# Kernel tuning notes

Measured on AMD Instinct MI355X. Metric: run time of the kernel, lower is better.

The kernel has to match this reference:

```python
import jax, jax.numpy as jnp
import numpy as np

N_NODES = 100000
N_EDGES = 1600000
D_IN = 64
D_OUT = 64


def setup_inputs() -> dict:
    key = jax.random.key(0)
    k1, k2, k3, k4, k5, k6 = jax.random.split(key, 6)
    feat = jax.random.normal(k1, (N_NODES, D_IN), dtype=jnp.float32)
    src = jax.random.randint(k2, (N_EDGES,), 0, N_NODES, dtype=jnp.int64)
    dst = jax.random.randint(k3, (N_EDGES,), 0, N_NODES, dtype=jnp.int64)
    edge_weight = jax.random.uniform(k4, (N_EDGES,), dtype=jnp.float32)
    # Xavier-uniform with relu gain, as in reset_parameters
    gain = float(np.sqrt(2.0))
    bound = gain * float(np.sqrt(6.0 / (D_IN + D_OUT)))
    W_neigh = jax.random.uniform(k5, (D_OUT, D_IN), dtype=jnp.float32, minval=-bound, maxval=bound)
    W_self = jax.random.uniform(k6, (D_OUT, D_IN), dtype=jnp.float32, minval=-bound, maxval=bound)
    bias = jnp.zeros((D_OUT,), dtype=jnp.float32)
    return {"feat": feat, "src": src, "dst": dst, "edge_weight": edge_weight,
            "W_neigh": W_neigh, "W_self": W_self, "bias": bias}


def reference(feat, src, dst, edge_weight, W_neigh, W_self, bias):
    n = feat.shape[0]
    # feat_drop with p=0.0 is identity; in_feats == out_feats so lin_before_mp is False
    # message: u_mul_e -> gather src features, scale by edge weight  [E, D_IN]
    m = feat[src] * edge_weight[:, None]
    # mean reduce over incoming edges (zero for isolated dst nodes, matching DGL)
    s = jax.ops.segment_sum(m, dst, num_segments=n)
    deg = jax.ops.segment_sum(jnp.ones_like(edge_weight), dst, num_segments=n)
    neigh = s / jnp.maximum(deg, 1.0)[:, None]
    h_neigh = neigh @ W_neigh.T
    h_self = feat @ W_self.T
    return h_self + h_neigh + bias
```

## Files before the change

kernel.cpp:

```cpp
#include <hip/hip_runtime.h>

constexpr int N_NODES = 100000;
constexpr int N_EDGES = 1600000;
constexpr int D = 64;

constexpr int BSH    = 7;
constexpr int BNODES = 1 << BSH;
constexpr int NBUCK  = (N_NODES + BNODES - 1) / BNODES;
constexpr int NPART  = 200;
constexpr int EPB    = N_EDGES / NPART;
constexpr int CAP    = 4096;

constexpr size_t OFF_BCNT    = 0;
constexpr size_t OFF_CURSOR  = 4096;
constexpr size_t OFF_BSTART  = 8192;
constexpr size_t OFF_STARTS  = 16384;
constexpr size_t OFF_ENTRIES = 425984;
constexpr size_t OFF_W16     = 13500416;
constexpr size_t OFF_AGG16   = 14680064;
constexpr size_t OFF_FEAT16  = 27480064;
constexpr size_t WS_NEEDED   = OFF_FEAT16 + (size_t)N_NODES * D * 2;

typedef short  bf16x8 __attribute__((ext_vector_type(8)));
typedef float  f32x4  __attribute__((ext_vector_type(4)));

__device__ __forceinline__ unsigned short f2bf(float f) {
    unsigned u = __float_as_uint(f);
    u += 0x7fffu + ((u >> 16) & 1u);
    return (unsigned short)(u >> 16);
}

__global__ __launch_bounds__(256) void k_cvt(const float4* __restrict__ feat4,
                                             unsigned short* __restrict__ feat16,
                                             const float* __restrict__ Wn,
                                             const float* __restrict__ Ws,
                                             unsigned short* __restrict__ W16) {
    const int i = blockIdx.x * 256 + threadIdx.x;
    float4 v = feat4[i];
    ushort4 o;
    o.x = f2bf(v.x); o.y = f2bf(v.y); o.z = f2bf(v.z); o.w = f2bf(v.w);
    *(ushort4*)&feat16[(size_t)i * 4] = o;
    if (blockIdx.x == 0) {
        for (int e = threadIdx.x; e < D * 128; e += 256) {
            const int j = e >> 7, k = e & 127;
            const float w = (k < D) ? Ws[j * D + k] : Wn[j * D + (k - D)];
            W16[e] = f2bf(w);
        }
    }
}

__global__ __launch_bounds__(256) void k_zero(int* __restrict__ bcnt) {
    int i = blockIdx.x * 256 + threadIdx.x;
    if (i < NBUCK) bcnt[i] = 0;
}

__global__ __launch_bounds__(256) void k_bcount(const int* __restrict__ dst,
                                                int* __restrict__ bcnt) {
    __shared__ int l[NBUCK];
    const int tid  = threadIdx.x;
    const int base = blockIdx.x * EPB;
    for (int i = tid; i < NBUCK; i += 256) l[i] = 0;
    __syncthreads();
    for (int k = tid; k < EPB; k += 256)
        atomicAdd(&l[dst[base + k] >> BSH], 1);
    __syncthreads();
    for (int b = tid; b < NBUCK; b += 256)
        if (l[b]) atomicAdd(&bcnt[b], l[b]);
}

__global__ __launch_bounds__(1024) void k_scan(const int* __restrict__ bcnt,
                                               int* __restrict__ bstart,
                                               int* __restrict__ cursor,
                                               int* __restrict__ starts) {
    __shared__ int s[1024];
    const int tid = threadIdx.x;
    const int v = (tid < NBUCK) ? bcnt[tid] : 0;
    s[tid] = v;
    __syncthreads();
    for (int off = 1; off < 1024; off <<= 1) {
        int u = (tid >= off) ? s[tid - off] : 0;
        __syncthreads();
        s[tid] += u;
        __syncthreads();
    }
    const int excl = s[tid] - v;
    if (tid <= NBUCK) bstart[tid] = excl;
    if (tid < NBUCK)  cursor[tid] = excl;
    if (tid == 0)     starts[N_NODES] = N_EDGES;
}

__global__ __launch_bounds__(256) void k_part(const int* __restrict__ src,
                                              const int* __restrict__ dst,
                                              const float* __restrict__ ew,
                                              int* __restrict__ cursor,
                                              uint2* __restrict__ entries) {
    __shared__ int l[NBUCK];
    const int tid  = threadIdx.x;
    const int base = blockIdx.x * EPB;
    for (int i = tid; i < NBUCK; i += 256) l[i] = 0;
    __syncthreads();
    for (int k = tid; k < EPB; k += 256)
        atomicAdd(&l[dst[base + k] >> BSH], 1);
    __syncthreads();
    for (int b = tid; b < NBUCK; b += 256) {
        const int c = l[b];
        l[b] = c ? atomicAdd(&cursor[b], c) : 0;
    }
    __syncthreads();
    for (int k = tid; k < EPB; k += 256) {
        const int e = base + k;
        const int d = dst[e];
        const int pos = atomicAdd(&l[d >> BSH], 1);
        entries[pos] = make_uint2((unsigned)src[e] | ((unsigned)(d & (BNODES - 1)) << 17),
                                  __float_as_uint(ew[e]));
    }
}

__global__ __launch_bounds__(256) void k_sort(uint2* __restrict__ entries,
                                              const int* __restrict__ bstart,
                                              int* __restrict__ starts) {
    __shared__ uint2 ent[CAP];
    __shared__ int h[BNODES];
    __shared__ int sc[BNODES];
    __shared__ int cur[BNODES];
    const int tid = threadIdx.x;
    const int b   = blockIdx.x;
    const int s0  = bstart[b];
    const int s1  = bstart[b + 1];
    const int cnt = (s1 - s0 <= CAP) ? (s1 - s0) : CAP;

    for (int i = tid; i < BNODES; i += 256) h[i] = 0;
    __syncthreads();
    for (int i = tid; i < cnt; i += 256) {
        uint2 e = entries[s0 + i];
        ent[i] = e;
        atomicAdd(&h[(e.x >> 17) & (BNODES - 1)], 1);
    }
    __syncthreads();
    if (tid < BNODES) sc[tid] = h[tid];
    __syncthreads();
    for (int off = 1; off < BNODES; off <<= 1) {
        int u = 0;
        if (tid < BNODES && tid >= off) u = sc[tid - off];
        __syncthreads();
        if (tid < BNODES) sc[tid] += u;
        __syncthreads();
    }
    if (tid < BNODES) {
        const int excl = sc[tid] - h[tid];
        cur[tid] = excl;
        const int node = (b << BSH) + tid;
        if (node < N_NODES) starts[node] = s0 + excl;
    }
    __syncthreads();
    for (int i = tid; i < cnt; i += 256) {
        uint2 e = ent[i];
        const int pos = atomicAdd(&cur[(e.x >> 17) & (BNODES - 1)], 1);
        entries[s0 + pos] = e;
    }
}

__global__ __launch_bounds__(256) void k_agg(const uint2* __restrict__ feat16u2,
                                             const int* __restrict__ starts,
                                             const uint2* __restrict__ entries,
                                             uint2* __restrict__ agg16u2) {
    const int wave = threadIdx.x >> 6;
    const int lane = threadIdx.x & 63;
    const int n = blockIdx.x * 4 + wave;
    if (n >= N_NODES) return;
    const int group = lane >> 4;
    const int gl    = lane & 15;
    const int s0 = starts[n];
    const int s1 = starts[n + 1];

    float4 acc = make_float4(0.f, 0.f, 0.f, 0.f);
    for (int e = s0 + group; e < s1; e += 4) {
        const uint2 en = entries[e];
        const float w  = __uint_as_float(en.y);
        const uint2 p  = feat16u2[(size_t)(en.x & 0x1FFFF) * 16 + gl];
        acc.x = fmaf(__uint_as_float(p.x << 16),          w, acc.x);
        acc.y = fmaf(__uint_as_float(p.x & 0xFFFF0000u),  w, acc.y);
        acc.z = fmaf(__uint_as_float(p.y << 16),          w, acc.z);
        acc.w = fmaf(__uint_as_float(p.y & 0xFFFF0000u),  w, acc.w);
    }
#pragma unroll
    for (int m = 16; m <= 32; m <<= 1) {
        acc.x += __shfl_xor(acc.x, m);
        acc.y += __shfl_xor(acc.y, m);
        acc.z += __shfl_xor(acc.z, m);
        acc.w += __shfl_xor(acc.w, m);
    }
    if (group == 0) {
        const float inv = 1.0f / fmaxf((float)(s1 - s0), 1.0f);
        uint2 o;
        o.x = (unsigned)f2bf(acc.x * inv) | ((unsigned)f2bf(acc.y * inv) << 16);
        o.y = (unsigned)f2bf(acc.z * inv) | ((unsigned)f2bf(acc.w * inv) << 16);
        agg16u2[(size_t)n * 16 + gl] = o;
    }
}

__global__ __launch_bounds__(256) void k_final(const unsigned short* __restrict__ feat16,
                                               const unsigned short* __restrict__ agg16,
                                               const unsigned short* __restrict__ W16,
                                               const float* __restrict__ bias,
                                               float* __restrict__ out) {
    const int tid  = threadIdx.x;
    const int wave = tid >> 6, lane = tid & 63;
    const int quad = lane >> 4, r = lane & 15;
    const int node0 = blockIdx.x * 64 + wave * 16;
    int arow = node0 + r;
    if (arow > N_NODES - 1) arow = N_NODES - 1;

    bf16x8 a[4], b[4][4];
    a[0] = *(const bf16x8*)&feat16[(size_t)arow * 64 +      quad * 8];
    a[1] = *(const bf16x8*)&feat16[(size_t)arow * 64 + 32 + quad * 8];
    a[2] = *(const bf16x8*)&agg16 [(size_t)arow * 64 +      quad * 8];
    a[3] = *(const bf16x8*)&agg16 [(size_t)arow * 64 + 32 + quad * 8];
#pragma unroll
    for (int nt = 0; nt < 4; ++nt)
#pragma unroll
        for (int kc = 0; kc < 4; ++kc)
            b[nt][kc] = *(const bf16x8*)&W16[(size_t)(nt * 16 + r) * 128 + kc * 32 + quad * 8];

    f32x4 acc[4] = {};
#pragma unroll
    for (int kc = 0; kc < 4; ++kc)
#pragma unroll
        for (int nt = 0; nt < 4; ++nt)
            acc[nt] = __builtin_amdgcn_mfma_f32_16x16x32_bf16(a[kc], b[nt][kc], acc[nt], 0, 0, 0);

#pragma unroll
    for (int nt = 0; nt < 4; ++nt) {
        const float bv = bias[nt * 16 + r];
#pragma unroll
        for (int reg = 0; reg < 4; ++reg) {
            const int m = node0 + quad * 4 + reg;
            if (m < N_NODES) out[(size_t)m * 64 + nt * 16 + r] = acc[nt][reg] + bv;
        }
    }
}

__global__ __launch_bounds__(256) void fb_zero(float4* __restrict__ out4,
                                               float* __restrict__ deg) {
    const int stride = gridDim.x * blockDim.x;
    int i = blockIdx.x * blockDim.x + threadIdx.x;
    const int total4 = (N_NODES * D) / 4;
    for (int idx = i; idx < total4; idx += stride)
        out4[idx] = make_float4(0.f, 0.f, 0.f, 0.f);
    for (int idx = i; idx < N_NODES; idx += stride)
        deg[idx] = 0.f;
}

__global__ __launch_bounds__(256) void fb_scatter(
    const float* __restrict__ feat, const int* __restrict__ src,
    const int* __restrict__ dst, const float* __restrict__ ew,
    float* __restrict__ out, float* __restrict__ deg) {
    const int gid  = blockIdx.x * blockDim.x + threadIdx.x;
    const int e    = gid >> 6;
    const int lane = gid & 63;
    if (e >= N_EDGES) return;
    atomicAdd(&out[(size_t)dst[e] * D + lane], feat[(size_t)src[e] * D + lane] * ew[e]);
    if (lane == 0) atomicAdd(&deg[dst[e]], 1.0f);
}

__global__ __launch_bounds__(256) void fb_finalize(
    const float* __restrict__ feat, const float* __restrict__ Wn,
    const float* __restrict__ Ws, const float* __restrict__ bias,
    const float* __restrict__ deg, float* __restrict__ out) {
    __shared__ float lWn[D * 65];
    __shared__ float lWs[D * 65];
    for (int idx = threadIdx.x; idx < D * D; idx += 256) {
        const int r = idx >> 6, c = idx & 63;
        lWn[r * 65 + c] = Wn[idx];
        lWs[r * 65 + c] = Ws[idx];
    }
    __syncthreads();
    const int wave = threadIdx.x >> 6;
    const int lane = threadIdx.x & 63;
    const int n = blockIdx.x * 4 + wave;
    if (n >= N_NODES) return;
    const float f  = feat[(size_t)n * D + lane];
    const float sv = out[(size_t)n * D + lane];
    const float inv = 1.0f / fmaxf(deg[n], 1.0f);
    float acc_s = 0.f, acc_n = 0.f;
#pragma unroll
    for (int k = 0; k < D; ++k) {
        acc_s += __shfl(f, k)  * lWs[lane * 65 + k];
        acc_n += __shfl(sv, k) * lWn[lane * 65 + k];
    }
    out[(size_t)n * D + lane] = acc_s + acc_n * inv + bias[lane];
}

extern "C" void kernel_launch(void* const* d_in, const int* in_sizes, int n_in,
                              void* d_out, int out_size, void* d_ws, size_t ws_size,
                              hipStream_t stream) {
    const float* feat = (const float*)d_in[0];
    const int*   src  = (const int*)  d_in[1];
    const int*   dst  = (const int*)  d_in[2];
    const float* ew   = (const float*)d_in[3];
    const float* Wn   = (const float*)d_in[4];
    const float* Ws   = (const float*)d_in[5];
    const float* bias = (const float*)d_in[6];
    float* out = (float*)d_out;
    char* ws = (char*)d_ws;

    if (ws_size >= WS_NEEDED) {
        int*   bcnt    = (int*)(ws + OFF_BCNT);
        int*   cursor  = (int*)(ws + OFF_CURSOR);
        int*   bstart  = (int*)(ws + OFF_BSTART);
        int*   starts  = (int*)(ws + OFF_STARTS);
        uint2* entries = (uint2*)(ws + OFF_ENTRIES);
        unsigned short* W16    = (unsigned short*)(ws + OFF_W16);
        unsigned short* agg16  = (unsigned short*)(ws + OFF_AGG16);
        unsigned short* feat16 = (unsigned short*)(ws + OFF_FEAT16);

        k_cvt   <<<(N_NODES * D / 4 + 255) / 256, 256, 0, stream>>>(
                    (const float4*)feat, feat16, Wn, Ws, W16);
        k_zero  <<<(NBUCK + 255) / 256, 256, 0, stream>>>(bcnt);
        k_bcount<<<NPART, 256, 0, stream>>>(dst, bcnt);
        k_scan  <<<1, 1024, 0, stream>>>(bcnt, bstart, cursor, starts);
        k_part  <<<NPART, 256, 0, stream>>>(src, dst, ew, cursor, entries);
        k_sort  <<<NBUCK, 256, 0, stream>>>(entries, bstart, starts);
        k_agg   <<<(N_NODES + 3) / 4, 256, 0, stream>>>((const uint2*)feat16, starts,
                                                        entries, (uint2*)agg16);
        k_final <<<(N_NODES + 63) / 64, 256, 0, stream>>>(feat16, agg16, W16, bias, out);
    } else {
        float* deg = (float*)d_ws;
        fb_zero<<<2048, 256, 0, stream>>>((float4*)out, deg);
        fb_scatter<<<(N_EDGES * 64) / 256, 256, 0, stream>>>(feat, src, dst, ew, out, deg);
        fb_finalize<<<(N_NODES + 3) / 4, 256, 0, stream>>>(feat, Wn, Ws, bias, deg, out);
    }
}
```

Measured before the change: 249.1 us.

## Fuse bucket sort, aggregation and output GEMM into one per-bucket kernel

Buckets shrink to 64 destination nodes. One kernel now sorts each bucket's edges in shared memory, aggregates neighbour features into a shared-memory bf16 row buffer and runs the MFMA projection directly from it. This removes the separate sort, aggregate and final kernels along with the global round trips for sorted entries, per-node starts and the agg16 buffer. The feature conversion, weight conversion and bucket count are also merged into one launch. The trade-off is that each block processes 16 nodes per wave serially, which may lower parallelism, and the shared buffer now caps a bucket at 2048 edges.

```diff
diff --git a/kernel.cpp b/kernel.cpp
--- a/kernel.cpp
+++ b/kernel.cpp
@@ -4,25 +4,26 @@
 constexpr int N_EDGES = 1600000;
 constexpr int D = 64;
 
-constexpr int BSH    = 7;
-constexpr int BNODES = 1 << BSH;
-constexpr int NBUCK  = (N_NODES + BNODES - 1) / BNODES;
+constexpr int BSH    = 6;
+constexpr int BN     = 1 << BSH;
+constexpr int NBUCK  = (N_NODES + BN - 1) / BN;
 constexpr int NPART  = 200;
 constexpr int EPB    = N_EDGES / NPART;
-constexpr int CAP    = 4096;
+constexpr int CAP    = 2048;
+constexpr int NCVT   = (N_NODES * D / 4) / 256;
 
 constexpr size_t OFF_BCNT    = 0;
-constexpr size_t OFF_CURSOR  = 4096;
-constexpr size_t OFF_BSTART  = 8192;
-constexpr size_t OFF_STARTS  = 16384;
-constexpr size_t OFF_ENTRIES = 425984;
-constexpr size_t OFF_W16     = 13500416;
-constexpr size_t OFF_AGG16   = 14680064;
-constexpr size_t OFF_FEAT16  = 27480064;
+constexpr size_t OFF_CURSOR  = 8192;
+constexpr size_t OFF_BSTART  = 16384;
+constexpr size_t OFF_ENTRIES = 24576;
+constexpr size_t OFF_W16     = 24576 + (size_t)N_EDGES * 8;
+constexpr size_t OFF_FEAT16  = 12845056;
 constexpr size_t WS_NEEDED   = OFF_FEAT16 + (size_t)N_NODES * D * 2;
 
 typedef short  bf16x8 __attribute__((ext_vector_type(8)));
 typedef float  f32x4  __attribute__((ext_vector_type(4)));
+
+union FragU { unsigned u[4]; bf16x8 v; };
 
 __device__ __forceinline__ unsigned short f2bf(float f) {
     unsigned u = __float_as_uint(f);
@@ -30,18 +31,38 @@
     return (unsigned short)(u >> 16);
 }
 
-__global__ __launch_bounds__(256) void k_cvt(const float4* __restrict__ feat4,
+__global__ __launch_bounds__(256) void k_zero(int* __restrict__ bcnt) {
+    int i = blockIdx.x * 256 + threadIdx.x;
+    if (i < NBUCK) bcnt[i] = 0;
+}
+
+__global__ __launch_bounds__(256) void k_pre(const float4* __restrict__ feat4,
                                              unsigned short* __restrict__ feat16,
                                              const float* __restrict__ Wn,
                                              const float* __restrict__ Ws,
-                                             unsigned short* __restrict__ W16) {
-    const int i = blockIdx.x * 256 + threadIdx.x;
-    float4 v = feat4[i];
-    ushort4 o;
-    o.x = f2bf(v.x); o.y = f2bf(v.y); o.z = f2bf(v.z); o.w = f2bf(v.w);
-    *(ushort4*)&feat16[(size_t)i * 4] = o;
-    if (blockIdx.x == 0) {
-        for (int e = threadIdx.x; e < D * 128; e += 256) {
+                                             unsigned short* __restrict__ W16,
+                                             const int* __restrict__ dst,
+                                             int* __restrict__ bcnt) {
+    __shared__ int l[NBUCK];
+    const int b   = blockIdx.x;
+    const int tid = threadIdx.x;
+    if (b < NCVT) {
+        const int i = b * 256 + tid;
+        float4 v = feat4[i];
+        ushort4 o;
+        o.x = f2bf(v.x); o.y = f2bf(v.y); o.z = f2bf(v.z); o.w = f2bf(v.w);
+        *(ushort4*)&feat16[(size_t)i * 4] = o;
+    } else if (b < NCVT + NPART) {
+        const int base = (b - NCVT) * EPB;
+        for (int i = tid; i < NBUCK; i += 256) l[i] = 0;
+        __syncthreads();
+        for (int k = tid; k < EPB; k += 256)
+            atomicAdd(&l[dst[base + k] >> BSH], 1);
+        __syncthreads();
+        for (int i = tid; i < NBUCK; i += 256)
+            if (l[i]) atomicAdd(&bcnt[i], l[i]);
+    } else {
+        for (int e = tid; e < D * 128; e += 256) {
             const int j = e >> 7, k = e & 127;
             const float w = (k < D) ? Ws[j * D + k] : Wn[j * D + (k - D)];
             W16[e] = f2bf(w);
@@ -49,44 +70,27 @@
     }
 }
 
-__global__ __launch_bounds__(256) void k_zero(int* __restrict__ bcnt) {
-    int i = blockIdx.x * 256 + threadIdx.x;
-    if (i < NBUCK) bcnt[i] = 0;
-}
-
-__global__ __launch_bounds__(256) void k_bcount(const int* __restrict__ dst,
-                                                int* __restrict__ bcnt) {
-    __shared__ int l[NBUCK];
-    const int tid  = threadIdx.x;
-    const int base = blockIdx.x * EPB;
-    for (int i = tid; i < NBUCK; i += 256) l[i] = 0;
-    __syncthreads();
-    for (int k = tid; k < EPB; k += 256)
-        atomicAdd(&l[dst[base + k] >> BSH], 1);
-    __syncthreads();
-    for (int b = tid; b < NBUCK; b += 256)
-        if (l[b]) atomicAdd(&bcnt[b], l[b]);
-}
-
 __global__ __launch_bounds__(1024) void k_scan(const int* __restrict__ bcnt,
                                                int* __restrict__ bstart,
-                                               int* __restrict__ cursor,
-                                               int* __restrict__ starts) {
+                                               int* __restrict__ cursor) {
     __shared__ int s[1024];
-    const int tid = threadIdx.x;
-    const int v = (tid < NBUCK) ? bcnt[tid] : 0;
-    s[tid] = v;
+    const int t  = threadIdx.x;
+    const int i0 = 2 * t, i1 = 2 * t + 1;
+    const int c0 = (i0 < NBUCK) ? bcnt[i0] : 0;
+    const int c1 = (i1 < NBUCK) ? bcnt[i1] : 0;
+    const int v  = c0 + c1;
+    s[t] = v;
     __syncthreads();
     for (int off = 1; off < 1024; off <<= 1) {
-        int u = (tid >= off) ? s[tid - off] : 0;
-        __syncthreads();
-        s[tid] += u;
-        __syncthreads();
-    }
-    const int excl = s[tid] - v;
-    if (tid <= NBUCK) bstart[tid] = excl;
-    if (tid < NBUCK)  cursor[tid] = excl;
-    if (tid == 0)     starts[N_NODES] = N_EDGES;
+        int u = (t >= off) ? s[t - off] : 0;
+        __syncthreads();
+        s[t] += u;
+        __syncthreads();
+    }
+    const int excl = s[t] - v;
+    if (i0 < NBUCK) { bstart[i0] = excl;      cursor[i0] = excl; }
+    if (i1 < NBUCK) { bstart[i1] = excl + c0; cursor[i1] = excl + c0; }
+    if (t == 0) bstart[NBUCK] = N_EDGES;
 }
 
 __global__ __launch_bounds__(256) void k_part(const int* __restrict__ src,
@@ -111,123 +115,116 @@
         const int e = base + k;
         const int d = dst[e];
         const int pos = atomicAdd(&l[d >> BSH], 1);
-        entries[pos] = make_uint2((unsigned)src[e] | ((unsigned)(d & (BNODES - 1)) << 17),
+        entries[pos] = make_uint2((unsigned)src[e] | ((unsigned)(d & (BN - 1)) << 17),
                                   __float_as_uint(ew[e]));
     }
 }
 
-__global__ __launch_bounds__(256) void k_sort(uint2* __restrict__ entries,
-                                              const int* __restrict__ bstart,
-                                              int* __restrict__ starts) {
+__global__ __launch_bounds__(256) void k_bucket(const uint2* __restrict__ feat16u2,
+                                                const unsigned short* __restrict__ feat16,
+                                                const int* __restrict__ bstart,
+                                                const uint2* __restrict__ entries,
+                                                const unsigned short* __restrict__ W16,
+                                                const float* __restrict__ bias,
+                                                float* __restrict__ out) {
     __shared__ uint2 ent[CAP];
-    __shared__ int h[BNODES];
-    __shared__ int sc[BNODES];
-    __shared__ int cur[BNODES];
+    __shared__ __align__(16) uint2 aggrow[BN * 16];
+    __shared__ int hh[BN], st[BN], cur[BN];
     const int tid = threadIdx.x;
     const int b   = blockIdx.x;
     const int s0  = bstart[b];
-    const int s1  = bstart[b + 1];
-    const int cnt = (s1 - s0 <= CAP) ? (s1 - s0) : CAP;
-
-    for (int i = tid; i < BNODES; i += 256) h[i] = 0;
+    int cnt = bstart[b + 1] - s0;
+    if (cnt > CAP) cnt = CAP;
+
+    if (tid < BN) hh[tid] = 0;
+    __syncthreads();
+    for (int i = tid; i < cnt; i += 256)
+        atomicAdd(&hh[(entries[s0 + i].x >> 17) & (BN - 1)], 1);
+    __syncthreads();
+    if (tid < BN) st[tid] = hh[tid];
+    __syncthreads();
+    for (int off = 1; off < BN; off <<= 1) {
+        int u = 0;
+        if (tid < BN && tid >= off) u = st[tid - off];
+        __syncthreads();
+        if (tid < BN) st[tid] += u;
+        __syncthreads();
+    }
+    if (tid < BN) { const int e0 = st[tid] - hh[tid]; st[tid] = e0; cur[tid] = e0; }
     __syncthreads();
     for (int i = tid; i < cnt; i += 256) {
         uint2 e = entries[s0 + i];
-        ent[i] = e;
-        atomicAdd(&h[(e.x >> 17) & (BNODES - 1)], 1);
-    }
-    __syncthreads();
-    if (tid < BNODES) sc[tid] = h[tid];
-    __syncthreads();
-    for (int off = 1; off < BNODES; off <<= 1) {
-        int u = 0;
-        if (tid < BNODES && tid >= off) u = sc[tid - off];
-        __syncthreads();
-        if (tid < BNODES) sc[tid] += u;
-        __syncthreads();
-    }
-    if (tid < BNODES) {
-        const int excl = sc[tid] - h[tid];
-        cur[tid] = excl;
-        const int node = (b << BSH) + tid;
-        if (node < N_NODES) starts[node] = s0 + excl;
-    }
-    __syncthreads();
-    for (int i = tid; i < cnt; i += 256) {
-        uint2 e = ent[i];
-        const int pos = atomicAdd(&cur[(e.x >> 17) & (BNODES - 1)], 1);
-        entries[s0 + pos] = e;
-    }
-}
-
-__global__ __launch_bounds__(256) void k_agg(const uint2* __restrict__ feat16u2,
-                                             const int* __restrict__ starts,
-                                             const uint2* __restrict__ entries,
-                                             uint2* __restrict__ agg16u2) {
-    const int wave = threadIdx.x >> 6;
-    const int lane = threadIdx.x & 63;
-    const int n = blockIdx.x * 4 + wave;
-    if (n >= N_NODES) return;
-    const int group = lane >> 4;
-    const int gl    = lane & 15;
-    const int s0 = starts[n];
-    const int s1 = starts[n + 1];
-
-    float4 acc = make_float4(0.f, 0.f, 0.f, 0.f);
-    for (int e = s0 + group; e < s1; e += 4) {
-        const uint2 en = entries[e];
-        const float w  = __uint_as_float(en.y);
-        const uint2 p  = feat16u2[(size_t)(en.x & 0x1FFFF) * 16 + gl];
-        acc.x = fmaf(__uint_as_float(p.x << 16),          w, acc.x);
-        acc.y = fmaf(__uint_as_float(p.x & 0xFFFF0000u),  w, acc.y);
-        acc.z = fmaf(__uint_as_float(p.y << 16),          w, acc.z);
-        acc.w = fmaf(__uint_as_float(p.y & 0xFFFF0000u),  w, acc.w);
-    }
-#pragma unroll
-    for (int m = 16; m <= 32; m <<= 1) {
-        acc.x += __shfl_xor(acc.x, m);
-        acc.y += __shfl_xor(acc.y, m);
-        acc.z += __shfl_xor(acc.z, m);
-        acc.w += __shfl_xor(acc.w, m);
-    }
-    if (group == 0) {
-        const float inv = 1.0f / fmaxf((float)(s1 - s0), 1.0f);
-        uint2 o;
-        o.x = (unsigned)f2bf(acc.x * inv) | ((unsigned)f2bf(acc.y * inv) << 16);
-        o.y = (unsigned)f2bf(acc.z * inv) | ((unsigned)f2bf(acc.w * inv) << 16);
-        agg16u2[(size_t)n * 16 + gl] = o;
-    }
-}
-
-__global__ __launch_bounds__(256) void k_final(const unsigned short* __restrict__ feat16,
-                                               const unsigned short* __restrict__ agg16,
-                                               const unsigned short* __restrict__ W16,
-                                               const float* __restrict__ bias,
-                                               float* __restrict__ out) {
-    const int tid  = threadIdx.x;
+        const int pos = atomicAdd(&cur[(e.x >> 17) & (BN - 1)], 1);
+        ent[pos] = e;
+    }
+    __syncthreads();
+
     const int wave = tid >> 6, lane = tid & 63;
+    const int group = lane >> 4, gl = lane & 15;
+    for (int t = 0; t < 16; ++t) {
+        const int dl  = wave * 16 + t;
+        const int ss  = st[dl];
+        const int deg = hh[dl];
+        const int se  = ss + deg;
+        float4 acc = make_float4(0.f, 0.f, 0.f, 0.f);
+        for (int e = ss + group; e < se; e += 4) {
+            const uint2 en = ent[e];
+            const float w  = __uint_as_float(en.y);
+            const uint2 p  = feat16u2[(size_t)(en.x & 0x1FFFF) * 16 + gl];
+            acc.x = fmaf(__uint_as_float(p.x << 16),         w, acc.x);
+            acc.y = fmaf(__uint_as_float(p.x & 0xFFFF0000u), w, acc.y);
+            acc.z = fmaf(__uint_as_float(p.y << 16),         w, acc.z);
+            acc.w = fmaf(__uint_as_float(p.y & 0xFFFF0000u), w, acc.w);
+        }
+#pragma unroll
+        for (int m = 16; m <= 32; m <<= 1) {
+            acc.x += __shfl_xor(acc.x, m);
+            acc.y += __shfl_xor(acc.y, m);
+            acc.z += __shfl_xor(acc.z, m);
+            acc.w += __shfl_xor(acc.w, m);
+        }
+        if (group == 0) {
+            const float inv = 1.0f / fmaxf((float)deg, 1.0f);
+            uint2 o;
+            o.x = (unsigned)f2bf(acc.x * inv) | ((unsigned)f2bf(acc.y * inv) << 16);
+            o.y = (unsigned)f2bf(acc.z * inv) | ((unsigned)f2bf(acc.w * inv) << 16);
+            aggrow[dl * 16 + gl] = o;
+        }
+    }
+    __syncthreads();
+
     const int quad = lane >> 4, r = lane & 15;
-    const int node0 = blockIdx.x * 64 + wave * 16;
+    const int node0 = b * BN + wave * 16;
     int arow = node0 + r;
     if (arow > N_NODES - 1) arow = N_NODES - 1;
 
-    bf16x8 a[4], b[4][4];
+    bf16x8 a[4], bb[4][4];
     a[0] = *(const bf16x8*)&feat16[(size_t)arow * 64 +      quad * 8];
     a[1] = *(const bf16x8*)&feat16[(size_t)arow * 64 + 32 + quad * 8];
-    a[2] = *(const bf16x8*)&agg16 [(size_t)arow * 64 +      quad * 8];
-    a[3] = *(const bf16x8*)&agg16 [(size_t)arow * 64 + 32 + quad * 8];
+    {
+        const int rbase = (wave * 16 + r) * 16;
+        FragU f2, f3;
+        uint2 lo = aggrow[rbase + 2 * quad];
+        uint2 hi = aggrow[rbase + 2 * quad + 1];
+        f2.u[0] = lo.x; f2.u[1] = lo.y; f2.u[2] = hi.x; f2.u[3] = hi.y;
+        lo = aggrow[rbase + 8 + 2 * quad];
+        hi = aggrow[rbase + 8 + 2 * quad + 1];
+        f3.u[0] = lo.x; f3.u[1] = lo.y; f3.u[2] = hi.x; f3.u[3] = hi.y;
+        a[2] = f2.v;
+        a[3] = f3.v;
+    }
 #pragma unroll
     for (int nt = 0; nt < 4; ++nt)
 #pragma unroll
         for (int kc = 0; kc < 4; ++kc)
-            b[nt][kc] = *(const bf16x8*)&W16[(size_t)(nt * 16 + r) * 128 + kc * 32 + quad * 8];
+            bb[nt][kc] = *(const bf16x8*)&W16[(size_t)(nt * 16 + r) * 128 + kc * 32 + quad * 8];
 
     f32x4 acc[4] = {};
 #pragma unroll
     for (int kc = 0; kc < 4; ++kc)
 #pragma unroll
         for (int nt = 0; nt < 4; ++nt)
-            acc[nt] = __builtin_amdgcn_mfma_f32_16x16x32_bf16(a[kc], b[nt][kc], acc[nt], 0, 0, 0);
+            acc[nt] = __builtin_amdgcn_mfma_f32_16x16x32_bf16(a[kc], bb[nt][kc], acc[nt], 0, 0, 0);
 
 #pragma unroll
     for (int nt = 0; nt < 4; ++nt) {
@@ -308,22 +305,17 @@
         int*   bcnt    = (int*)(ws + OFF_BCNT);
         int*   cursor  = (int*)(ws + OFF_CURSOR);
         int*   bstart  = (int*)(ws + OFF_BSTART);
-        int*   starts  = (int*)(ws + OFF_STARTS);
         uint2* entries = (uint2*)(ws + OFF_ENTRIES);
         unsigned short* W16    = (unsigned short*)(ws + OFF_W16);
-        unsigned short* agg16  = (unsigned short*)(ws + OFF_AGG16);
         unsigned short* feat16 = (unsigned short*)(ws + OFF_FEAT16);
 
-        k_cvt   <<<(N_NODES * D / 4 + 255) / 256, 256, 0, stream>>>(
-                    (const float4*)feat, feat16, Wn, Ws, W16);
         k_zero  <<<(NBUCK + 255) / 256, 256, 0, stream>>>(bcnt);
-        k_bcount<<<NPART, 256, 0, stream>>>(dst, bcnt);
-        k_scan  <<<1, 1024, 0, stream>>>(bcnt, bstart, cursor, starts);
+        k_pre   <<<NCVT + NPART + 1, 256, 0, stream>>>((const float4*)feat, feat16,
+                                                       Wn, Ws, W16, dst, bcnt);
+        k_scan  <<<1, 1024, 0, stream>>>(bcnt, bstart, cursor);
         k_part  <<<NPART, 256, 0, stream>>>(src, dst, ew, cursor, entries);
-        k_sort  <<<NBUCK, 256, 0, stream>>>(entries, bstart, starts);
-        k_agg   <<<(N_NODES + 3) / 4, 256, 0, stream>>>((const uint2*)feat16, starts,
-                                                        entries, (uint2*)agg16);
-        k_final <<<(N_NODES + 63) / 64, 256, 0, stream>>>(feat16, agg16, W16, bias, out);
+        k_bucket<<<NBUCK, 256, 0, stream>>>((const uint2*)feat16, feat16, bstart,
+                                            entries, W16, bias, out);
     } else {
         float* deg = (float*)d_ws;
         fb_zero<<<2048, 256, 0, stream>>>((float4*)out, deg);
```

New measurement: 234.3 us. 5.9% less time.
